# Kernel tuning notes

Hardware: AMD Instinct MI355X
Metric: run time of the kernel (lower is better)

The kernel has to match this reference:

```python
import jax, jax.numpy as jnp
import numpy as np

B, SEG, P, H, NH = 8, 16, 256, 1024, 16
DH = H // NH
T = P + 1                 # tokens per segment (segment lord + segment_size)
L = 1 + SEG * T           # 4113
LN_EPS = 1e-12


def setup_inputs() -> dict:
    key = jax.random.key(0)
    ks = jax.random.split(key, 9)
    s = 0.02
    return {
        "hidden_states": jax.random.normal(ks[0], (B, L, H), jnp.float32),
        "Blord_w": jax.random.normal(ks[1], (H, H), jnp.float32) * s,
        "Blord_b": jnp.zeros((H,), jnp.float32),
        "seg_qw": jax.random.normal(ks[2], (SEG, H, H), jnp.float32) * s,
        "seg_kw": jax.random.normal(ks[3], (SEG, H, H), jnp.float32) * s,
        "seg_vw": jax.random.normal(ks[4], (SEG, H, H), jnp.float32) * s,
        "lord_qw": jax.random.normal(ks[5], (H, H), jnp.float32) * s,
        "lord_kw": jax.random.normal(ks[6], (H, H), jnp.float32) * s,
        "lord_vw": jax.random.normal(ks[7], (H, H), jnp.float32) * s,
        "out_w": jax.random.normal(ks[8], (H, H), jnp.float32) * s,
        "out_b": jnp.zeros((H,), jnp.float32),
        "ln_w": jnp.ones((H,), jnp.float32),
        "ln_b": jnp.zeros((H,), jnp.float32),
    }


def reference(hidden_states, Blord_w, Blord_b, seg_qw, seg_kw, seg_vw,
              lord_qw, lord_kw, lord_vw, out_w, out_b, ln_w, ln_b):
    scale = 1.0 / np.sqrt(DH).astype(np.float32)

    # global lord projection of token 0 (torch Linear: x @ W.T + b)
    Blord = hidden_states[:, 0] @ Blord_w.T + Blord_b              # [B,H]

    # per-segment local full attention (each segment has its own QKV weights)
    seg_x = hidden_states[:, 1:].reshape(B, SEG, T, H)             # [B,S,T,H]
    q = jnp.einsum('bsti,soi->bsto', seg_x, seg_qw).reshape(B, SEG, T, NH, DH)
    k = jnp.einsum('bsti,soi->bsto', seg_x, seg_kw).reshape(B, SEG, T, NH, DH)
    v = jnp.einsum('bsti,soi->bsto', seg_x, seg_vw).reshape(B, SEG, T, NH, DH)
    scores = jnp.einsum('bsqhd,bskhd->bshqk', q, k) * scale        # [B,S,NH,T,T]
    probs = jax.nn.softmax(scores, axis=-1)
    seg_out = jnp.einsum('bshqk,bskhd->bsqhd', probs, v).reshape(B, SEG, T, H)

    # global attention over lord tokens: [Blord, seg_out[:, :, 0]]
    lords_in = jnp.concatenate([Blord[:, None, :], seg_out[:, :, 0, :]], axis=1)  # [B,S+1,H]
    lq = (lords_in @ lord_qw.T).reshape(B, SEG + 1, NH, DH)
    lk = (lords_in @ lord_kw.T).reshape(B, SEG + 1, NH, DH)
    lv = (lords_in @ lord_vw.T).reshape(B, SEG + 1, NH, DH)
    lscores = jnp.einsum('bqhd,bkhd->bhqk', lq, lk) * scale        # [B,NH,S+1,S+1]
    lprobs = jax.nn.softmax(lscores, axis=-1)
    lords = jnp.einsum('bhqk,bkhd->bqhd', lprobs, lv).reshape(B, SEG + 1, H)

    # reassemble: global lord, then per segment (updated lord token, local tokens)
    seg_out = seg_out.at[:, :, 0, :].set(lords[:, 1:])
    self_outputs = jnp.concatenate(
        [lords[:, :1], seg_out.reshape(B, SEG * T, H)], axis=1)    # [B,L,H]

    # output dense + residual + LayerNorm
    h = self_outputs @ out_w.T + out_b + hidden_states
    mu = h.mean(axis=-1, keepdims=True)
    var = h.var(axis=-1, keepdims=True)
    attention_output = (h - mu) / jnp.sqrt(var + LN_EPS) * ln_w + ln_b
    return attention_output, self_outputs
```

## Files before the change

### kernel.cpp

```cpp
#include <hip/hip_runtime.h>
#include <hip/hip_bf16.h>

typedef long long ll;
typedef __attribute__((ext_vector_type(8))) short bf16x8;
typedef __attribute__((ext_vector_type(4))) float fx4;

#define B_ 8
#define SEG_ 16
#define T_ 257
#define H_ 1024
#define NH_ 16
#define L_ 4113
#define SCALE 0.125f

__device__ __forceinline__ unsigned short f2bfu(float x) {
  __hip_bfloat16 h = __float2bfloat16(x);
  return *(unsigned short*)&h;
}

__device__ __forceinline__ void gl_lds16(const void* g, void* l) {
  __builtin_amdgcn_global_load_lds((const __attribute__((address_space(1))) void*)g,
                                   (__attribute__((address_space(3))) void*)l, 16, 0, 0);
}

#define NU_HID 4211712
#define NU_W   2097152
#define NU_OW  131072
__global__ __launch_bounds__(256) void f2bf_all(
    const float* __restrict__ hid, __hip_bfloat16* __restrict__ hbf,
    const float* __restrict__ wq, const float* __restrict__ wk, const float* __restrict__ wv,
    __hip_bfloat16* __restrict__ w3,
    const float* __restrict__ ow, __hip_bfloat16* __restrict__ owb)
{
  const int NTOT = NU_HID + 3 * NU_W + NU_OW;
  for (int i = blockIdx.x * 256 + threadIdx.x; i < NTOT; i += gridDim.x * 256) {
    const float* src;
    __hip_bfloat16* dst;
    if (i < NU_HID) {
      src = hid + (ll)i * 8;
      dst = hbf + (ll)i * 8;
    } else if (i < NU_HID + 3 * NU_W) {
      int j = i - NU_HID;
      int which = j >> 21;
      int off = j & (NU_W - 1);
      const float* ws = (which == 0) ? wq : (which == 1) ? wk : wv;
      src = ws + (ll)off * 8;
      dst = w3 + (ll)j * 8;
    } else {
      int k = i - NU_HID - 3 * NU_W;
      src = ow + (ll)k * 8;
      dst = owb + (ll)k * 8;
    }
    float4 a = ((const float4*)src)[0];
    float4 b = ((const float4*)src)[1];
    union { bf16x8 v; unsigned short u[8]; } o;
    o.u[0] = f2bfu(a.x); o.u[1] = f2bfu(a.y); o.u[2] = f2bfu(a.z); o.u[3] = f2bfu(a.w);
    o.u[4] = f2bfu(b.x); o.u[5] = f2bfu(b.y); o.u[6] = f2bfu(b.z); o.u[7] = f2bfu(b.w);
    *(bf16x8*)dst = o.v;
  }
}

__global__ __launch_bounds__(256) void gemm_qkv(
    const __hip_bfloat16* __restrict__ A,
    const __hip_bfloat16* __restrict__ Wall,
    __hip_bfloat16* __restrict__ Cq,
    __hip_bfloat16* __restrict__ Ck,
    __hip_bfloat16* __restrict__ Cv)
{
  const int nwg = 24 * 17 * 16;
  const int orig = blockIdx.x + 24 * (blockIdx.y + 17 * blockIdx.z);
  const int swz = (orig & 7) * (nwg >> 3) + (orig >> 3);
  const int bx = swz % 24;
  const int t2 = swz / 24;
  const int by = t2 % 17;
  const int bz = t2 / 17;
  const int which = bx >> 3;
  const int n0 = (bx & 7) * 128;
  const int m0 = by * 128;
  const int M = B_ * T_;

  const __hip_bfloat16* W = Wall + ((ll)which * SEG_ + bz) * ((ll)H_ * H_);
  __hip_bfloat16* C = (which == 0) ? Cq : (which == 1) ? Ck : Cv;

  __shared__ __hip_bfloat16 At[3][128 * 32];
  __shared__ __hip_bfloat16 Bt[3][128 * 32];

  const int tid = threadIdx.x;
  const int lane = tid & 63;
  const int wid = tid >> 6;
  const int wm = (wid >> 1) * 64;
  const int wn = (wid & 1) * 64;

  const int r0 = tid >> 2;
  const int p = tid & 3;
  const int kc  = p * 8;
  const int kcs = (p ^ ((r0 >> 1) & 3)) * 8;
  const int am0 = min(m0 + r0, M - 1);
  const int am1 = min(m0 + 64 + r0, M - 1);
  const ll segoff = (ll)bz * ((ll)T_ * H_);
  const ll aoff0 = (ll)(am0 / T_) * ((ll)L_ * H_) + segoff + (ll)(am0 % T_) * H_;
  const ll aoff1 = (ll)(am1 / T_) * ((ll)L_ * H_) + segoff + (ll)(am1 % T_) * H_;
  const ll boff0 = (ll)(n0 + r0) * H_;
  const ll boff1 = (ll)(n0 + 64 + r0) * H_;
  const int stA0 = r0 * 32 + kc;

  fx4 acc[4][4];
#pragma unroll
  for (int i = 0; i < 4; ++i)
#pragma unroll
    for (int j = 0; j < 4; ++j) acc[i][j] = fx4{0.f, 0.f, 0.f, 0.f};

  const int sw = ((lane & 15) >> 1) & 3;
  const int fragA = (wm + (lane & 15)) * 32 + (((lane >> 4) ^ sw) << 3);
  const int fragB = (wn + (lane & 15)) * 32 + (((lane >> 4) ^ sw) << 3);

#define STAGE_QKV(buf, kt) do { const int kk = (kt) * 32; \
    gl_lds16(A + aoff0 + kk + kcs, (void*)(&At[buf][0] + stA0)); \
    gl_lds16(A + aoff1 + kk + kcs, (void*)(&At[buf][0] + 2048 + stA0)); \
    gl_lds16(W + boff0 + kk + kcs, (void*)(&Bt[buf][0] + stA0)); \
    gl_lds16(W + boff1 + kk + kcs, (void*)(&Bt[buf][0] + 2048 + stA0)); } while (0)

  STAGE_QKV(0, 0);
  STAGE_QKV(1, 1);
  for (int t = 0; t < 32; ++t) {
    __builtin_amdgcn_s_barrier();
    asm volatile("" ::: "memory");
    if (t + 2 < 32) { const int b3 = (t + 2) % 3; STAGE_QKV(b3, t + 2); }
    if (t < 30)       asm volatile("s_waitcnt vmcnt(8)" ::: "memory");
    else if (t == 30) asm volatile("s_waitcnt vmcnt(4)" ::: "memory");
    else              asm volatile("s_waitcnt vmcnt(0)" ::: "memory");
    __builtin_amdgcn_s_barrier();
    asm volatile("" ::: "memory");

    const int cb = t % 3;
    const __hip_bfloat16* ap = &At[cb][0] + fragA;
    const __hip_bfloat16* bp = &Bt[cb][0] + fragB;
    bf16x8 af[4], bfr[4];
#pragma unroll
    for (int f = 0; f < 4; ++f) {
      af[f]  = *(const bf16x8*)(ap + f * 16 * 32);
      bfr[f] = *(const bf16x8*)(bp + f * 16 * 32);
    }
#pragma unroll
    for (int mf = 0; mf < 4; ++mf)
#pragma unroll
      for (int nf = 0; nf < 4; ++nf)
        acc[mf][nf] = __builtin_amdgcn_mfma_f32_16x16x32_bf16(af[mf], bfr[nf], acc[mf][nf], 0, 0, 0);
  }
#undef STAGE_QKV

  const int cn = n0 + wn + (lane & 15);
#pragma unroll
  for (int mf = 0; mf < 4; ++mf) {
    int mloc = m0 + wm + mf * 16 + ((lane >> 4) << 2);
#pragma unroll
    for (int r = 0; r < 4; ++r) {
      int m = mloc + r;
      if (m >= M) continue;
      ll co = ((ll)(m / T_) * SEG_ + bz) * ((ll)T_ * H_) + (ll)(m % T_) * H_;
#pragma unroll
      for (int nf = 0; nf < 4; ++nf)
        C[co + cn + nf * 16] = __float2bfloat16(acc[mf][nf][r]);
    }
  }
}

__global__ __launch_bounds__(256) void gemm_out(
    const __hip_bfloat16* __restrict__ A,
    const __hip_bfloat16* __restrict__ W,
    const float* __restrict__ bias,
    float* __restrict__ C,
    const float* __restrict__ res)
{
  const int nwg = 8 * 258;
  const int orig = blockIdx.x + 8 * blockIdx.y;
  const int swz = (orig & 7) * (nwg >> 3) + (orig >> 3);
  const int bx = swz % 8;
  const int by = swz / 8;
  const int M = B_ * L_;
  const int m0 = by * 128;
  const int n0 = bx * 128;

  __shared__ __hip_bfloat16 At[3][128 * 32];
  __shared__ __hip_bfloat16 Bt[3][128 * 32];

  const int tid = threadIdx.x;
  const int lane = tid & 63;
  const int wid = tid >> 6;
  const int wm = (wid >> 1) * 64;
  const int wn = (wid & 1) * 64;

  const int r0 = tid >> 2;
  const int p = tid & 3;
  const int kc  = p * 8;
  const int kcs = (p ^ ((r0 >> 1) & 3)) * 8;
  const ll aoff0 = (ll)min(m0 + r0, M - 1) * H_;
  const ll aoff1 = (ll)min(m0 + 64 + r0, M - 1) * H_;
  const ll boff0 = (ll)(n0 + r0) * H_;
  const ll boff1 = (ll)(n0 + 64 + r0) * H_;
  const int stA0 = r0 * 32 + kc;

  fx4 acc[4][4];
#pragma unroll
  for (int i = 0; i < 4; ++i)
#pragma unroll
    for (int j = 0; j < 4; ++j) acc[i][j] = fx4{0.f, 0.f, 0.f, 0.f};

  const int sw = ((lane & 15) >> 1) & 3;
  const int fragA = (wm + (lane & 15)) * 32 + (((lane >> 4) ^ sw) << 3);
  const int fragB = (wn + (lane & 15)) * 32 + (((lane >> 4) ^ sw) << 3);

#define STAGE_O(buf, kt) do { const int kk = (kt) * 32; \
    gl_lds16(A + aoff0 + kk + kcs, (void*)(&At[buf][0] + stA0)); \
    gl_lds16(A + aoff1 + kk + kcs, (void*)(&At[buf][0] + 2048 + stA0)); \
    gl_lds16(W + boff0 + kk + kcs, (void*)(&Bt[buf][0] + stA0)); \
    gl_lds16(W + boff1 + kk + kcs, (void*)(&Bt[buf][0] + 2048 + stA0)); } while (0)

  STAGE_O(0, 0);
  STAGE_O(1, 1);
  for (int t = 0; t < 32; ++t) {
    __builtin_amdgcn_s_barrier();
    asm volatile("" ::: "memory");
    if (t + 2 < 32) { const int b3 = (t + 2) % 3; STAGE_O(b3, t + 2); }
    if (t < 30)       asm volatile("s_waitcnt vmcnt(8)" ::: "memory");
    else if (t == 30) asm volatile("s_waitcnt vmcnt(4)" ::: "memory");
    else              asm volatile("s_waitcnt vmcnt(0)" ::: "memory");
    __builtin_amdgcn_s_barrier();
    asm volatile("" ::: "memory");

    const int cb = t % 3;
    const __hip_bfloat16* ap = &At[cb][0] + fragA;
    const __hip_bfloat16* bp = &Bt[cb][0] + fragB;
    bf16x8 af[4], bfr[4];
#pragma unroll
    for (int f = 0; f < 4; ++f) {
      af[f]  = *(const bf16x8*)(ap + f * 16 * 32);
      bfr[f] = *(const bf16x8*)(bp + f * 16 * 32);
    }
#pragma unroll
    for (int mf = 0; mf < 4; ++mf)
#pragma unroll
      for (int nf = 0; nf < 4; ++nf)
        acc[mf][nf] = __builtin_amdgcn_mfma_f32_16x16x32_bf16(af[mf], bfr[nf], acc[mf][nf], 0, 0, 0);
  }
#undef STAGE_O

  const int cn = n0 + wn + (lane & 15);
#pragma unroll
  for (int mf = 0; mf < 4; ++mf) {
    int mloc = m0 + wm + mf * 16 + ((lane >> 4) << 2);
#pragma unroll
    for (int r = 0; r < 4; ++r) {
      int m = mloc + r;
      if (m >= M) continue;
#pragma unroll
      for (int nf = 0; nf < 4; ++nf) {
        int n = cn + nf * 16;
        C[(ll)m * H_ + n] = acc[mf][nf][r] + bias[n] + res[(ll)m * H_ + n];
      }
    }
  }
}

__global__ __launch_bounds__(256) void seg_attn_mfma(
    const __hip_bfloat16* __restrict__ Qb,
    const __hip_bfloat16* __restrict__ Kb,
    const __hip_bfloat16* __restrict__ Vb,
    float* __restrict__ so, __hip_bfloat16* __restrict__ sob)
{
  __shared__ __align__(16) char smem[8192 + 9216 + 4 * 4096];
  char* KsB = smem;
  char* VTB = smem + 8192;
  const int tid = threadIdx.x, lane = tid & 63, wid = tid >> 6;
  char* PB = smem + 8192 + 9216 + wid * 4096;

  const int h = blockIdx.y, bs = blockIdx.z;
  const int b = bs >> 4, s = bs & 15;
  const int q0 = blockIdx.x * 128 + wid * 32;
  const bool qvalid = (q0 <= 256);
  const ll base = (ll)bs * (T_ * H_) + h * 64;

  bf16x8 qf[2][2];
#pragma unroll
  for (int mf = 0; mf < 2; ++mf) {
    int qr = q0 + mf * 16 + (lane & 15); if (qr > 256) qr = 256;
#pragma unroll
    for (int ks = 0; ks < 2; ++ks)
      qf[mf][ks] = *(const bf16x8*)(Qb + base + (ll)qr * H_ + ks * 32 + ((lane >> 4) << 3));
  }

  float l_[2][4];
  fx4 of[2][4];
#pragma unroll
  for (int mf = 0; mf < 2; ++mf) {
#pragma unroll
    for (int r = 0; r < 4; ++r) l_[mf][r] = 0.f;
#pragma unroll
    for (int df = 0; df < 4; ++df) of[mf][df] = fx4{0.f, 0.f, 0.f, 0.f};
  }

  const int krow = tid >> 3;
  const int kc8 = tid & 7;
  const int kkp = tid & 31;
  const int vd0 = (tid >> 5) * 8;

  for (int t = 0; t < 5; ++t) {
    const int k0 = t * 64;
    __syncthreads();
    {
      int row = krow;
      int kr = k0 + row; if (kr > 256) kr = 256;
      gl_lds16(Kb + base + (ll)kr * H_ + ((kc8 ^ (row & 7)) << 3), KsB + tid * 16);
      row = krow + 32;
      kr = k0 + row; if (kr > 256) kr = 256;
      gl_lds16(Kb + base + (ll)kr * H_ + ((kc8 ^ (row & 7)) << 3), KsB + 4096 + tid * 16);
    }
    {
      int kk = kkp * 2;
      int kr0 = k0 + kk;     if (kr0 > 256) kr0 = 256;
      int kr1 = k0 + kk + 1; if (kr1 > 256) kr1 = 256;
      bf16x8 v0 = *(const bf16x8*)(Vb + base + (ll)kr0 * H_ + vd0);
      bf16x8 v1 = *(const bf16x8*)(Vb + base + (ll)kr1 * H_ + vd0);
      unsigned int* vtu = (unsigned int*)VTB;
#pragma unroll
      for (int j = 0; j < 8; ++j)
        vtu[(vd0 + j) * 36 + kkp] =
            (unsigned int)(unsigned short)v0[j] | ((unsigned int)(unsigned short)v1[j] << 16);
    }
    __syncthreads();

    if (qvalid) {
      fx4 sa[2][4];
#pragma unroll
      for (int mf = 0; mf < 2; ++mf)
#pragma unroll
        for (int nf = 0; nf < 4; ++nf) sa[mf][nf] = fx4{0.f, 0.f, 0.f, 0.f};
#pragma unroll
      for (int nf = 0; nf < 4; ++nf) {
        int key = nf * 16 + (lane & 15);
#pragma unroll
        for (int ks = 0; ks < 2; ++ks) {
          int c16 = ks * 4 + (lane >> 4);
          bf16x8 kf = *(const bf16x8*)(KsB + key * 128 + ((c16 ^ (key & 7)) << 4));
          sa[0][nf] = __builtin_amdgcn_mfma_f32_16x16x32_bf16(qf[0][ks], kf, sa[0][nf], 0, 0, 0);
          sa[1][nf] = __builtin_amdgcn_mfma_f32_16x16x32_bf16(qf[1][ks], kf, sa[1][nf], 0, 0, 0);
        }
      }
#pragma unroll
      for (int nf = 0; nf < 4; ++nf) {
        bool bad = (k0 + nf * 16 + (lane & 15)) > 256;
#pragma unroll
        for (int mf = 0; mf < 2; ++mf) {
#pragma unroll
          for (int r = 0; r < 4; ++r) {
            float pexp = bad ? 0.f : __expf(sa[mf][nf][r] * SCALE);
            sa[mf][nf][r] = pexp;
            l_[mf][r] += pexp;
          }
        }
      }
#pragma unroll
      for (int mf = 0; mf < 2; ++mf)
#pragma unroll
        for (int nf = 0; nf < 4; ++nf)
#pragma unroll
          for (int rp = 0; rp < 2; ++rp) {
            float v0 = sa[mf][nf][rp];
            float v2 = sa[mf][nf][rp + 2];
            float o0 = __shfl_xor(v0, 1);
            float o2 = __shfl_xor(v2, 1);
            const bool odd = (lane & 1);
            float lo = odd ? o2 : v0;
            float hi = odd ? v2 : o0;
            unsigned int pk = (unsigned int)f2bfu(lo) | ((unsigned int)f2bfu(hi) << 16);
            int row = mf * 16 + ((lane >> 4) << 2) + (odd ? rp + 2 : rp);
            int col2 = nf * 16 + (lane & 14);
            *(unsigned int*)(PB + row * 128 + ((col2 * 2) ^ ((row & 7) << 4))) = pk;
          }
#pragma unroll
      for (int kks = 0; kks < 2; ++kks) {
        bf16x8 pa[2];
#pragma unroll
        for (int mf = 0; mf < 2; ++mf) {
          int prow = mf * 16 + (lane & 15);
          int c16 = kks * 4 + (lane >> 4);
          pa[mf] = *(const bf16x8*)(PB + prow * 128 + ((c16 ^ (prow & 7)) << 4));
        }
#pragma unroll
        for (int df = 0; df < 4; ++df) {
          bf16x8 vf = *(const bf16x8*)(VTB + (df * 16 + (lane & 15)) * 144 + kks * 64 + ((lane >> 4) << 4));
          of[0][df] = __builtin_amdgcn_mfma_f32_16x16x32_bf16(pa[0], vf, of[0][df], 0, 0, 0);
          of[1][df] = __builtin_amdgcn_mfma_f32_16x16x32_bf16(pa[1], vf, of[1][df], 0, 0, 0);
        }
      }
    }
  }

  if (qvalid) {
#pragma unroll
    for (int mf = 0; mf < 2; ++mf)
#pragma unroll
      for (int r = 0; r < 4; ++r) {
        float rs = l_[mf][r];
        rs += __shfl_xor(rs, 1);
        rs += __shfl_xor(rs, 2);
        rs += __shfl_xor(rs, 4);
        rs += __shfl_xor(rs, 8);
        l_[mf][r] = rs;
      }
#pragma unroll
    for (int mf = 0; mf < 2; ++mf)
#pragma unroll
      for (int r = 0; r < 4; ++r) {
        int q = q0 + mf * 16 + ((lane >> 4) << 2) + r;
        if (q > 256) continue;
        float inv = 1.f / l_[mf][r];
        ll rowoff = ((ll)b * L_ + 1 + (ll)s * T_ + q) * H_ + h * 64;
#pragma unroll
        for (int df = 0; df < 4; ++df) {
          int d = df * 16 + (lane & 15);
          float v = of[mf][df][r] * inv;
          so[rowoff + d] = v;
          sob[rowoff + d] = __float2bfloat16(v);
        }
      }
  }
}

__global__ __launch_bounds__(256) void gemm_bt(
    const float* __restrict__ X, ll xbs,
    const float* __restrict__ W,
    const float* __restrict__ bias,
    float* __restrict__ C, ll cbs,
    int M, int K)
{
  const int tid = threadIdx.x;
  const int n0 = blockIdx.x * 64;

  __shared__ float Xt[16][68];
  __shared__ float Wt[16][68];

  const int lr = tid >> 2;
  const int lc = (tid & 3) << 2;
  const int mload = min(lr, M - 1);
  const ll xoff = (ll)mload * xbs;
  const ll woff = (ll)(n0 + lr) * K;

  const int tr = tid >> 4;
  const int tc = tid & 15;

  float acc[4][4];
#pragma unroll
  for (int i = 0; i < 4; ++i)
#pragma unroll
    for (int j = 0; j < 4; ++j) acc[i][j] = 0.f;

  for (int k0 = 0; k0 < K; k0 += 16) {
    float4 xv = *(const float4*)(X + xoff + k0 + lc);
    float4 wv = *(const float4*)(W + woff + k0 + lc);
    __syncthreads();
    Xt[lc + 0][lr] = xv.x; Xt[lc + 1][lr] = xv.y; Xt[lc + 2][lr] = xv.z; Xt[lc + 3][lr] = xv.w;
    Wt[lc + 0][lr] = wv.x; Wt[lc + 1][lr] = wv.y; Wt[lc + 2][lr] = wv.z; Wt[lc + 3][lr] = wv.w;
    __syncthreads();
#pragma unroll
    for (int kk = 0; kk < 16; ++kk) {
      float4 xa = *(const float4*)&Xt[kk][tr << 2];
      float4 wb = *(const float4*)&Wt[kk][tc << 2];
      float xa_[4] = {xa.x, xa.y, xa.z, xa.w};
      float wb_[4] = {wb.x, wb.y, wb.z, wb.w};
#pragma unroll
      for (int i = 0; i < 4; ++i)
#pragma unroll
        for (int j = 0; j < 4; ++j)
          acc[i][j] = fmaf(xa_[i], wb_[j], acc[i][j]);
    }
  }

#pragma unroll
  for (int i = 0; i < 4; ++i) {
    int m = (tr << 2) + i;
    if (m >= M) continue;
#pragma unroll
    for (int j = 0; j < 4; ++j) {
      int n = n0 + (tc << 2) + j;
      C[(ll)m * cbs + n] = acc[i][j] + (bias ? bias[n] : 0.f);
    }
  }
}

__global__ __launch_bounds__(256) void lord_proj(
    const float* __restrict__ X,
    const float* __restrict__ Wq, const float* __restrict__ Wk, const float* __restrict__ Wv,
    float* __restrict__ Cq, float* __restrict__ Ck, float* __restrict__ Cv)
{
  const float* W = (blockIdx.z == 0) ? Wq : (blockIdx.z == 1) ? Wk : Wv;
  float* C = (blockIdx.z == 0) ? Cq : (blockIdx.z == 1) ? Ck : Cv;
  const int M = 136, K = 1024;

  const int tid = threadIdx.x;
  const int m0 = blockIdx.y * 64;
  const int n0 = blockIdx.x * 64;

  __shared__ float Xt[16][68];
  __shared__ float Wt[16][68];

  const int lr = tid >> 2;
  const int lc = (tid & 3) << 2;
  const int mload = min(m0 + lr, M - 1);
  const ll xoff = (ll)mload * K;
  const ll woff = (ll)(n0 + lr) * K;

  const int tr = tid >> 4;
  const int tc = tid & 15;

  float acc[4][4];
#pragma unroll
  for (int i = 0; i < 4; ++i)
#pragma unroll
    for (int j = 0; j < 4; ++j) acc[i][j] = 0.f;

  for (int k0 = 0; k0 < K; k0 += 16) {
    float4 xv = *(const float4*)(X + xoff + k0 + lc);
    float4 wv = *(const float4*)(W + woff + k0 + lc);
    __syncthreads();
    Xt[lc + 0][lr] = xv.x; Xt[lc + 1][lr] = xv.y; Xt[lc + 2][lr] = xv.z; Xt[lc + 3][lr] = xv.w;
    Wt[lc + 0][lr] = wv.x; Wt[lc + 1][lr] = wv.y; Wt[lc + 2][lr] = wv.z; Wt[lc + 3][lr] = wv.w;
    __syncthreads();
#pragma unroll
    for (int kk = 0; kk < 16; ++kk) {
      float4 xa = *(const float4*)&Xt[kk][tr << 2];
      float4 wb = *(const float4*)&Wt[kk][tc << 2];
      float xa_[4] = {xa.x, xa.y, xa.z, xa.w};
      float wb_[4] = {wb.x, wb.y, wb.z, wb.w};
#pragma unroll
      for (int i = 0; i < 4; ++i)
#pragma unroll
        for (int j = 0; j < 4; ++j)
          acc[i][j] = fmaf(xa_[i], wb_[j], acc[i][j]);
    }
  }

#pragma unroll
  for (int i = 0; i < 4; ++i) {
    int m = m0 + (tr << 2) + i;
    if (m >= M) continue;
#pragma unroll
    for (int j = 0; j < 4; ++j)
      C[(ll)m * 1024 + n0 + (tc << 2) + j] = acc[i][j];
  }
}

__global__ __launch_bounds__(256) void copy_lords_in(
    const float* __restrict__ so, float* __restrict__ lin)
{
  int b = blockIdx.x / SEG_, s = blockIdx.x % SEG_;
  int i = threadIdx.x * 4;
  *(float4*)(lin + ((ll)(b * 17 + 1 + s)) * H_ + i) =
      *(const float4*)(so + ((ll)b * L_ + 1 + (ll)s * T_) * H_ + i);
}

__global__ __launch_bounds__(256) void lord_attn2(
    const float* __restrict__ lq, const float* __restrict__ lk,
    const float* __restrict__ lv, float* __restrict__ so,
    __hip_bfloat16* __restrict__ sob)
{
  const int b = blockIdx.x, h = blockIdx.y;
  const int tid = threadIdx.x, lane = tid & 63, wid = tid >> 6;
  __shared__ float Qs[17][64], Ks[17][64], Vs[17][64];
  for (int t = tid; t < 17 * 64; t += 256) {
    int r = t >> 6, c = t & 63;
    ll g = ((ll)(b * 17 + r)) * H_ + h * 64 + c;
    Qs[r][c] = lq[g];
    Ks[r][c] = lk[g];
    Vs[r][c] = lv[g];
  }
  __syncthreads();
  for (int q = wid; q < 17; q += 4) {
    float qd = Qs[q][lane];
    float sc[17];
#pragma unroll
    for (int k = 0; k < 17; ++k) {
      float p = qd * Ks[k][lane];
      p += __shfl_xor(p, 1);  p += __shfl_xor(p, 2);  p += __shfl_xor(p, 4);
      p += __shfl_xor(p, 8);  p += __shfl_xor(p, 16); p += __shfl_xor(p, 32);
      sc[k] = p * SCALE;
    }
    float mx = sc[0];
#pragma unroll
    for (int k = 1; k < 17; ++k) mx = fmaxf(mx, sc[k]);
    float l = 0.f;
#pragma unroll
    for (int k = 0; k < 17; ++k) { sc[k] = __expf(sc[k] - mx); l += sc[k]; }
    float invl = 1.f / l;
    float o = 0.f;
#pragma unroll
    for (int k = 0; k < 17; ++k) o = fmaf(sc[k], Vs[k][lane], o);
    o *= invl;
    ll row = (q == 0) ? (ll)b * L_ : ((ll)b * L_ + 1 + (ll)(q - 1) * T_);
    so[row * H_ + h * 64 + lane] = o;
    sob[row * H_ + h * 64 + lane] = __float2bfloat16(o);
  }
}

__global__ __launch_bounds__(256) void ln_inplace(
    float* __restrict__ hbuf, const float* __restrict__ w, const float* __restrict__ bgain)
{
  const ll row = blockIdx.x;
  const int tid = threadIdx.x;
  float4 x = *(float4*)(hbuf + row * H_ + tid * 4);
  float s = x.x + x.y + x.z + x.w;
  float s2 = x.x * x.x + x.y * x.y + x.z * x.z + x.w * x.w;
#pragma unroll
  for (int off = 32; off >= 1; off >>= 1) {
    s  += __shfl_down(s, off, 64);
    s2 += __shfl_down(s2, off, 64);
  }
  __shared__ float red[2][4];
  int wid = tid >> 6;
  if ((tid & 63) == 0) { red[0][wid] = s; red[1][wid] = s2; }
  __syncthreads();
  s  = red[0][0] + red[0][1] + red[0][2] + red[0][3];
  s2 = red[1][0] + red[1][1] + red[1][2] + red[1][3];
  const float mean = s * (1.f / H_);
  float var = s2 * (1.f / H_) - mean * mean;
  var = fmaxf(var, 0.f);
  const float inv = rsqrtf(var + 1e-12f);
  float4 g = *(const float4*)(w + tid * 4);
  float4 bb = *(const float4*)(bgain + tid * 4);
  float4 y;
  y.x = (x.x - mean) * inv * g.x + bb.x;
  y.y = (x.y - mean) * inv * g.y + bb.y;
  y.z = (x.z - mean) * inv * g.z + bb.z;
  y.w = (x.w - mean) * inv * g.w + bb.w;
  *(float4*)(hbuf + row * H_ + tid * 4) = y;
}

extern "C" void kernel_launch(void* const* d_in, const int* in_sizes, int n_in,
                              void* d_out, int out_size, void* d_ws, size_t ws_size,
                              hipStream_t stream)
{
  const float* hidden  = (const float*)d_in[0];
  const float* Blord_w = (const float*)d_in[1];
  const float* Blord_b = (const float*)d_in[2];
  const float* seg_qw  = (const float*)d_in[3];
  const float* seg_kw  = (const float*)d_in[4];
  const float* seg_vw  = (const float*)d_in[5];
  const float* lord_qw = (const float*)d_in[6];
  const float* lord_kw = (const float*)d_in[7];
  const float* lord_vw = (const float*)d_in[8];
  const float* out_w   = (const float*)d_in[9];
  const float* out_b   = (const float*)d_in[10];
  const float* ln_w    = (const float*)d_in[11];
  const float* ln_b    = (const float*)d_in[12];

  float* attn_out = (float*)d_out;
  float* self_out = (float*)d_out + (ll)B_ * L_ * H_;

  const ll QKV = (ll)B_ * SEG_ * T_ * H_;
  const ll SHH = (ll)SEG_ * H_ * H_;
  __hip_bfloat16* qb = (__hip_bfloat16*)attn_out;
  __hip_bfloat16* kb = qb + QKV;
  __hip_bfloat16* hbf = (__hip_bfloat16*)self_out;
  __hip_bfloat16* vb = (__hip_bfloat16*)d_ws;
  __hip_bfloat16* wslot3 = vb + QKV;
  __hip_bfloat16* sob = wslot3;
  __hip_bfloat16* outw_bf = wslot3 + 3 * SHH;
  float* lords_in = (float*)(outw_bf + (ll)H_ * H_);
  float* lqw_ = lords_in + 136 * 1024;
  float* lkw_ = lqw_ + 136 * 1024;
  float* lvw_ = lkw_ + 136 * 1024;

  dim3 blk(256);

  f2bf_all<<<dim3(2048), blk, 0, stream>>>(
      hidden, hbf, seg_qw, seg_kw, seg_vw, wslot3, out_w, outw_bf);

  gemm_qkv<<<dim3(24, 17, 16), blk, 0, stream>>>(hbf + H_, wslot3, qb, kb, vb);

  gemm_bt<<<dim3(16), blk, 0, stream>>>(
      hidden, (ll)L_ * H_, Blord_w, Blord_b, lords_in, (ll)17 * H_, B_, H_);

  seg_attn_mfma<<<dim3(3, NH_, B_ * SEG_), blk, 0, stream>>>(qb, kb, vb, self_out, sob);

  copy_lords_in<<<dim3(B_ * SEG_), blk, 0, stream>>>(self_out, lords_in);

  lord_proj<<<dim3(16, 3, 3), blk, 0, stream>>>(
      lords_in, lord_qw, lord_kw, lord_vw, lqw_, lkw_, lvw_);

  lord_attn2<<<dim3(B_, NH_), blk, 0, stream>>>(lqw_, lkw_, lvw_, self_out, sob);

  gemm_out<<<dim3(8, 258), blk, 0, stream>>>(sob, outw_bf, out_b, attn_out, hidden);

  ln_inplace<<<dim3(B_ * L_), blk, 0, stream>>>(attn_out, ln_w, ln_b);
}
```

Baseline: 851.1 us.

## Retile QKV GEMM to 256x256 blocks with 512 threads and 4-stage pipeline

Grows the per-segment QKV GEMM workgroup tile from 128x128 (256 threads) to 256x256 (512 threads, 8 waves each computing 128x64). This raises arithmetic intensity per LDS and global load. The LDS ring goes from 3 to 4 stages, with three tiles prefetched. The loop now needs one barrier per iteration instead of two, and MFMA issue is wrapped in s_setprio. In exchange, M padding grows (2056 rows into 9×256 tiles), LDS use rises to about 128KB, and there are fewer, heavier workgroups, which limits occupancy to one block per CU.

```diff
diff --git a/kernel.cpp b/kernel.cpp
--- a/kernel.cpp
+++ b/kernel.cpp
@@ -60,98 +60,104 @@
   }
 }
 
-__global__ __launch_bounds__(256) void gemm_qkv(
+__global__ __launch_bounds__(512) void gemm_qkv(
     const __hip_bfloat16* __restrict__ A,
     const __hip_bfloat16* __restrict__ Wall,
     __hip_bfloat16* __restrict__ Cq,
     __hip_bfloat16* __restrict__ Ck,
     __hip_bfloat16* __restrict__ Cv)
 {
-  const int nwg = 24 * 17 * 16;
-  const int orig = blockIdx.x + 24 * (blockIdx.y + 17 * blockIdx.z);
+  const int nwg = 12 * 9 * 16;
+  const int orig = blockIdx.x + 12 * (blockIdx.y + 9 * blockIdx.z);
   const int swz = (orig & 7) * (nwg >> 3) + (orig >> 3);
-  const int bx = swz % 24;
-  const int t2 = swz / 24;
-  const int by = t2 % 17;
-  const int bz = t2 / 17;
-  const int which = bx >> 3;
-  const int n0 = (bx & 7) * 128;
-  const int m0 = by * 128;
+  const int bx = swz % 12;
+  const int t2 = swz / 12;
+  const int by = t2 % 9;
+  const int bz = t2 / 9;
+  const int which = bx >> 2;
+  const int n0 = (bx & 3) * 256;
+  const int m0 = by * 256;
   const int M = B_ * T_;
 
   const __hip_bfloat16* W = Wall + ((ll)which * SEG_ + bz) * ((ll)H_ * H_);
   __hip_bfloat16* C = (which == 0) ? Cq : (which == 1) ? Ck : Cv;
 
-  __shared__ __hip_bfloat16 At[3][128 * 32];
-  __shared__ __hip_bfloat16 Bt[3][128 * 32];
+  __shared__ __hip_bfloat16 At[4][8192];
+  __shared__ __hip_bfloat16 Bt[4][8192];
 
   const int tid = threadIdx.x;
   const int lane = tid & 63;
   const int wid = tid >> 6;
-  const int wm = (wid >> 1) * 64;
-  const int wn = (wid & 1) * 64;
-
-  const int r0 = tid >> 2;
-  const int p = tid & 3;
-  const int kc  = p * 8;
-  const int kcs = (p ^ ((r0 >> 1) & 3)) * 8;
-  const int am0 = min(m0 + r0, M - 1);
-  const int am1 = min(m0 + 64 + r0, M - 1);
+  const int wm = (wid >> 2) * 128;
+  const int wn = (wid & 3) * 64;
+
+  const int rS = tid >> 2;
+  const int cS = tid & 3;
+  const int cs0 = (cS ^ ((rS >> 1) & 3)) * 8;
+  const int cs1 = (cS ^ (((rS + 128) >> 1) & 3)) * 8;
   const ll segoff = (ll)bz * ((ll)T_ * H_);
+  const int am0 = min(m0 + rS, M - 1);
+  const int am1 = min(m0 + 128 + rS, M - 1);
   const ll aoff0 = (ll)(am0 / T_) * ((ll)L_ * H_) + segoff + (ll)(am0 % T_) * H_;
   const ll aoff1 = (ll)(am1 / T_) * ((ll)L_ * H_) + segoff + (ll)(am1 % T_) * H_;
-  const ll boff0 = (ll)(n0 + r0) * H_;
-  const ll boff1 = (ll)(n0 + 64 + r0) * H_;
-  const int stA0 = r0 * 32 + kc;
-
-  fx4 acc[4][4];
-#pragma unroll
-  for (int i = 0; i < 4; ++i)
+  const ll boff0 = (ll)(n0 + rS) * H_;
+  const ll boff1 = (ll)(n0 + 128 + rS) * H_;
+
+  fx4 acc[8][4];
+#pragma unroll
+  for (int i = 0; i < 8; ++i)
 #pragma unroll
     for (int j = 0; j < 4; ++j) acc[i][j] = fx4{0.f, 0.f, 0.f, 0.f};
 
   const int sw = ((lane & 15) >> 1) & 3;
-  const int fragA = (wm + (lane & 15)) * 32 + (((lane >> 4) ^ sw) << 3);
-  const int fragB = (wn + (lane & 15)) * 32 + (((lane >> 4) ^ sw) << 3);
+  const int fragA0 = (wm + (lane & 15)) * 32 + (((lane >> 4) ^ sw) << 3);
+  const int fragB0 = (wn + (lane & 15)) * 32 + (((lane >> 4) ^ sw) << 3);
 
 #define STAGE_QKV(buf, kt) do { const int kk = (kt) * 32; \
-    gl_lds16(A + aoff0 + kk + kcs, (void*)(&At[buf][0] + stA0)); \
-    gl_lds16(A + aoff1 + kk + kcs, (void*)(&At[buf][0] + 2048 + stA0)); \
-    gl_lds16(W + boff0 + kk + kcs, (void*)(&Bt[buf][0] + stA0)); \
-    gl_lds16(W + boff1 + kk + kcs, (void*)(&Bt[buf][0] + 2048 + stA0)); } while (0)
+    gl_lds16(A + aoff0 + kk + cs0, (void*)(&At[buf][0] + tid * 8)); \
+    gl_lds16(A + aoff1 + kk + cs1, (void*)(&At[buf][0] + 4096 + tid * 8)); \
+    gl_lds16(W + boff0 + kk + cs0, (void*)(&Bt[buf][0] + tid * 8)); \
+    gl_lds16(W + boff1 + kk + cs1, (void*)(&Bt[buf][0] + 4096 + tid * 8)); } while (0)
 
   STAGE_QKV(0, 0);
   STAGE_QKV(1, 1);
+  STAGE_QKV(2, 2);
+  asm volatile("s_waitcnt vmcnt(8)" ::: "memory");
+  __builtin_amdgcn_s_barrier();
+  asm volatile("" ::: "memory");
+
   for (int t = 0; t < 32; ++t) {
-    __builtin_amdgcn_s_barrier();
-    asm volatile("" ::: "memory");
-    if (t + 2 < 32) { const int b3 = (t + 2) % 3; STAGE_QKV(b3, t + 2); }
-    if (t < 30)       asm volatile("s_waitcnt vmcnt(8)" ::: "memory");
-    else if (t == 30) asm volatile("s_waitcnt vmcnt(4)" ::: "memory");
-    else              asm volatile("s_waitcnt vmcnt(0)" ::: "memory");
-    __builtin_amdgcn_s_barrier();
-    asm volatile("" ::: "memory");
-
-    const int cb = t % 3;
-    const __hip_bfloat16* ap = &At[cb][0] + fragA;
-    const __hip_bfloat16* bp = &Bt[cb][0] + fragB;
-    bf16x8 af[4], bfr[4];
-#pragma unroll
-    for (int f = 0; f < 4; ++f) {
-      af[f]  = *(const bf16x8*)(ap + f * 16 * 32);
-      bfr[f] = *(const bf16x8*)(bp + f * 16 * 32);
-    }
-#pragma unroll
-    for (int mf = 0; mf < 4; ++mf)
+    if (t + 3 < 32) { STAGE_QKV((t + 3) & 3, t + 3); }
+
+    const __hip_bfloat16* ap = &At[t & 3][0] + fragA0;
+    const __hip_bfloat16* bp = &Bt[t & 3][0] + fragB0;
+    bf16x8 af[8], bfv[4];
+#pragma unroll
+    for (int mf = 0; mf < 8; ++mf) af[mf] = *(const bf16x8*)(ap + mf * 512);
+#pragma unroll
+    for (int nf = 0; nf < 4; ++nf) bfv[nf] = *(const bf16x8*)(bp + nf * 512);
+
+    __builtin_amdgcn_s_setprio(1);
+#pragma unroll
+    for (int mf = 0; mf < 8; ++mf)
 #pragma unroll
       for (int nf = 0; nf < 4; ++nf)
-        acc[mf][nf] = __builtin_amdgcn_mfma_f32_16x16x32_bf16(af[mf], bfr[nf], acc[mf][nf], 0, 0, 0);
+        acc[mf][nf] = __builtin_amdgcn_mfma_f32_16x16x32_bf16(af[mf], bfv[nf], acc[mf][nf], 0, 0, 0);
+    __builtin_amdgcn_s_setprio(0);
+
+    if (t < 31) {
+      if (t <= 28)      asm volatile("s_waitcnt vmcnt(8)" ::: "memory");
+      else if (t == 29) asm volatile("s_waitcnt vmcnt(4)" ::: "memory");
+      else              asm volatile("s_waitcnt vmcnt(0)" ::: "memory");
+      __builtin_amdgcn_s_barrier();
+      asm volatile("" ::: "memory");
+    }
   }
 #undef STAGE_QKV
 
   const int cn = n0 + wn + (lane & 15);
 #pragma unroll
-  for (int mf = 0; mf < 4; ++mf) {
+  for (int mf = 0; mf < 8; ++mf) {
     int mloc = m0 + wm + mf * 16 + ((lane >> 4) << 2);
 #pragma unroll
     for (int r = 0; r < 4; ++r) {
@@ -675,7 +681,7 @@
   f2bf_all<<<dim3(2048), blk, 0, stream>>>(
       hidden, hbf, seg_qw, seg_kw, seg_vw, wslot3, out_w, outw_bf);
 
-  gemm_qkv<<<dim3(24, 17, 16), blk, 0, stream>>>(hbf + H_, wslot3, qb, kb, vb);
+  gemm_qkv<<<dim3(12, 9, 16), dim3(512), 0, stream>>>(hbf + H_, wslot3, qb, kb, vb);
 
   gemm_bt<<<dim3(16), blk, 0, stream>>>(
       hidden, (ll)L_ * H_, Blord_w, Blord_b, lords_in, (ll)17 * H_, B_, H_);
```

Result: slower. 882.5 us (+3.7%).

## Split last query row of segment attention into a separate tail kernel

Applied to the files above, without the earlier changes.

The MFMA segment attention launched three query blocks per (head, segment), and the third block handled only query 256, wasting most of its work. It now launches two blocks covering queries 0-255 with no bounds checks, and a small 64-thread tail kernel computes the single remaining query row per head and segment with scalar math. The tail kernel has no running max in its softmax, so it relies on scores staying small. The QKV GEMM's workgroup swizzle decode is also reordered so neighbouring workgroups walk the M dimension first.

```diff
diff --git a/kernel.cpp b/kernel.cpp
--- a/kernel.cpp
+++ b/kernel.cpp
@@ -13,6 +13,9 @@
 #define L_ 4113
 #define SCALE 0.125f
 
+__device__ __forceinline__ float bf2f(unsigned short u) {
+  union { unsigned int i; float f; } w; w.i = ((unsigned int)u) << 16; return w.f;
+}
 __device__ __forceinline__ unsigned short f2bfu(float x) {
   __hip_bfloat16 h = __float2bfloat16(x);
   return *(unsigned short*)&h;
@@ -70,10 +73,10 @@
   const int nwg = 24 * 17 * 16;
   const int orig = blockIdx.x + 24 * (blockIdx.y + 17 * blockIdx.z);
   const int swz = (orig & 7) * (nwg >> 3) + (orig >> 3);
-  const int bx = swz % 24;
-  const int t2 = swz / 24;
-  const int by = t2 % 17;
-  const int bz = t2 / 17;
+  const int by = swz % 17;
+  const int tt = swz / 17;
+  const int bx = tt % 24;
+  const int bz = tt / 24;
   const int which = bx >> 3;
   const int n0 = (bx & 7) * 128;
   const int m0 = by * 128;
@@ -277,13 +280,12 @@
   const int h = blockIdx.y, bs = blockIdx.z;
   const int b = bs >> 4, s = bs & 15;
   const int q0 = blockIdx.x * 128 + wid * 32;
-  const bool qvalid = (q0 <= 256);
   const ll base = (ll)bs * (T_ * H_) + h * 64;
 
   bf16x8 qf[2][2];
 #pragma unroll
   for (int mf = 0; mf < 2; ++mf) {
-    int qr = q0 + mf * 16 + (lane & 15); if (qr > 256) qr = 256;
+    int qr = q0 + mf * 16 + (lane & 15);
 #pragma unroll
     for (int ks = 0; ks < 2; ++ks)
       qf[mf][ks] = *(const bf16x8*)(Qb + base + (ll)qr * H_ + ks * 32 + ((lane >> 4) << 3));
@@ -329,7 +331,7 @@
     }
     __syncthreads();
 
-    if (qvalid) {
+    {
       fx4 sa[2][4];
 #pragma unroll
       for (int mf = 0; mf < 2; ++mf)
@@ -396,7 +398,7 @@
     }
   }
 
-  if (qvalid) {
+  {
 #pragma unroll
     for (int mf = 0; mf < 2; ++mf)
 #pragma unroll
@@ -413,7 +415,6 @@
 #pragma unroll
       for (int r = 0; r < 4; ++r) {
         int q = q0 + mf * 16 + ((lane >> 4) << 2) + r;
-        if (q > 256) continue;
         float inv = 1.f / l_[mf][r];
         ll rowoff = ((ll)b * L_ + 1 + (ll)s * T_ + q) * H_ + h * 64;
 #pragma unroll
@@ -425,6 +426,72 @@
         }
       }
   }
+}
+
+__global__ __launch_bounds__(64) void seg_attn_tail(
+    const __hip_bfloat16* __restrict__ Qb,
+    const __hip_bfloat16* __restrict__ Kb,
+    const __hip_bfloat16* __restrict__ Vb,
+    float* __restrict__ so, __hip_bfloat16* __restrict__ sob)
+{
+  const int h = blockIdx.x & 15;
+  const int bs = blockIdx.x >> 4;
+  const int b = bs >> 4, s = bs & 15;
+  const int lane = threadIdx.x;
+  const ll base = (ll)bs * (T_ * H_) + h * 64;
+
+  __shared__ float qs[64];
+  __shared__ float osum[64][65];
+
+  if (lane < 8) {
+    bf16x8 qv = *(const bf16x8*)(Qb + base + (ll)256 * H_ + lane * 8);
+#pragma unroll
+    for (int j = 0; j < 8; ++j) qs[lane * 8 + j] = bf2f((unsigned short)qv[j]);
+  }
+  __syncthreads();
+
+  float l_part = 0.f;
+  float o[64];
+#pragma unroll
+  for (int d = 0; d < 64; ++d) o[d] = 0.f;
+
+  const int nk = (lane == 0) ? 5 : 4;
+  for (int kk = 0; kk < nk; ++kk) {
+    int key = (kk == 4) ? 256 : kk * 64 + lane;
+    const __hip_bfloat16* kp = Kb + base + (ll)key * H_;
+    const __hip_bfloat16* vp = Vb + base + (ll)key * H_;
+    float sc = 0.f;
+    float vv[64];
+#pragma unroll
+    for (int c = 0; c < 8; ++c) {
+      bf16x8 kv8 = *(const bf16x8*)(kp + c * 8);
+      bf16x8 vv8 = *(const bf16x8*)(vp + c * 8);
+#pragma unroll
+      for (int j = 0; j < 8; ++j) {
+        sc = fmaf(qs[c * 8 + j], bf2f((unsigned short)kv8[j]), sc);
+        vv[c * 8 + j] = bf2f((unsigned short)vv8[j]);
+      }
+    }
+    float pe = __expf(sc * SCALE);
+    l_part += pe;
+#pragma unroll
+    for (int d = 0; d < 64; ++d) o[d] = fmaf(pe, vv[d], o[d]);
+  }
+
+  float l = l_part;
+  l += __shfl_xor(l, 1);  l += __shfl_xor(l, 2);  l += __shfl_xor(l, 4);
+  l += __shfl_xor(l, 8);  l += __shfl_xor(l, 16); l += __shfl_xor(l, 32);
+
+#pragma unroll
+  for (int d = 0; d < 64; ++d) osum[lane][d] = o[d];
+  __syncthreads();
+  float od = 0.f;
+#pragma unroll
+  for (int r = 0; r < 64; ++r) od += osum[r][lane];
+  od /= l;
+  ll rowoff = ((ll)b * L_ + 1 + (ll)s * T_ + 256) * H_ + h * 64 + lane;
+  so[rowoff] = od;
+  sob[rowoff] = __float2bfloat16(od);
 }
 
 __global__ __launch_bounds__(256) void gemm_bt(
@@ -680,7 +747,8 @@
   gemm_bt<<<dim3(16), blk, 0, stream>>>(
       hidden, (ll)L_ * H_, Blord_w, Blord_b, lords_in, (ll)17 * H_, B_, H_);
 
-  seg_attn_mfma<<<dim3(3, NH_, B_ * SEG_), blk, 0, stream>>>(qb, kb, vb, self_out, sob);
+  seg_attn_mfma<<<dim3(2, NH_, B_ * SEG_), blk, 0, stream>>>(qb, kb, vb, self_out, sob);
+  seg_attn_tail<<<dim3(B_ * SEG_ * NH_), dim3(64), 0, stream>>>(qb, kb, vb, self_out, sob);
 
   copy_lords_in<<<dim3(B_ * SEG_), blk, 0, stream>>>(self_out, lords_in);
 
```

Measured after the change: 856.1 us. No clear change (+0.6%).
